# Kernel optimization log

Hardware: AMD Instinct MI355X
Metric: run time of the kernel (lower is better)

## Reference

```python
import jax, jax.numpy as jnp
import numpy as np

TEMPERATURE = 0.1
NORM_EPS = 1e-12  # matches torch F.normalize default eps


def setup_inputs() -> dict:
    key = jax.random.key(0)
    # [C crops, V=2 views, B batch, D out_dim]
    inp = jax.random.normal(key, (8, 2, 4096, 512), dtype=jnp.float32)
    return {"inp": inp}


def _ntxent_loss(inp, temperature=TEMPERATURE):
    # inp: [C, 2, B, D]
    C, V, B, D = inp.shape
    norm = jnp.linalg.norm(inp, axis=-1, keepdims=True)
    xn = inp / jnp.maximum(norm, NORM_EPS)  # l2-normalize each embedding

    # sim_all[i, b, j, v] = <xn[i,0,b], xn[j,v,b]> / temperature
    sim_all = jnp.einsum('ibd,jvbd->ibjv', xn[:, 0], xn) / temperature

    # positive logit: view-1 of the same crop i (label 0 in the original cat)
    sim_pos = sim_all[jnp.arange(C), :, jnp.arange(C), 1]  # [C, B]

    # negatives: both views of all crops j != i; mask out j == i with -inf
    same_crop = (jnp.arange(C)[:, None, None, None] == jnp.arange(C)[None, None, :, None])
    neg = jnp.where(same_crop, -jnp.inf, sim_all)  # [C, B, C, 2]

    # cross-entropy with label 0 == -log softmax over [pos, negs]
    all_logits = jnp.concatenate([sim_pos[..., None], neg.reshape(C, B, -1)], axis=-1)
    lse = jax.nn.logsumexp(all_logits, axis=-1)  # [C, B]
    loss_ib = lse - sim_pos

    # mean over crops i per sample, then mean over batch b
    return jnp.mean(loss_ib)


def reference(inp):
    return _ntxent_loss(inp)
```

## Files before the change

kernel.cpp:

```cpp
#include <hip/hip_runtime.h>
#include <hip/hip_bf16.h>
#include <math.h>

#define CC 8
#define BB 4096
#define DD 512
#define SLOT_STRIDE (BB * DD)

constexpr float INV_T    = 10.0f;
constexpr float NORM_EPS = 1e-12f;

typedef __attribute__((ext_vector_type(8))) short bf16x8;
typedef __attribute__((ext_vector_type(4))) float f32x4;

__device__ __forceinline__ short f2bf(float x) {
    union { __hip_bfloat16 h; short s; } u;
    u.h = __float2bfloat16(x);
    return u.s;
}

__global__ __launch_bounds__(256, 4)
void ntxent_mfma(const float* __restrict__ inp, float* __restrict__ partial) {
    const int lane = threadIdx.x & 63;
    const int wv   = threadIdx.x >> 6;
    const int b    = blockIdx.x * 4 + wv;
    const int slot = lane & 15;
    const int kg   = lane >> 4;

    const float4* p4 = reinterpret_cast<const float4*>(
        inp + (size_t)slot * SLOT_STRIDE + (size_t)b * DD);

    f32x4 acc0 = {0.f, 0.f, 0.f, 0.f};
    f32x4 acc1 = {0.f, 0.f, 0.f, 0.f};
    float n2a = 0.f, n2b = 0.f;

#pragma unroll
    for (int tt = 0; tt < 8; ++tt) {
#pragma unroll
        for (int h = 0; h < 2; ++h) {
            const int t = 2 * tt + h;
            const float4 lo = p4[8 * t + kg];
            const float4 hi = p4[8 * t + 4 + kg];
            n2a = fmaf(lo.x, lo.x, n2a);
            n2a = fmaf(lo.y, lo.y, n2a);
            n2a = fmaf(lo.z, lo.z, n2a);
            n2a = fmaf(lo.w, lo.w, n2a);
            n2b = fmaf(hi.x, hi.x, n2b);
            n2b = fmaf(hi.y, hi.y, n2b);
            n2b = fmaf(hi.z, hi.z, n2b);
            n2b = fmaf(hi.w, hi.w, n2b);
            bf16x8 f;
            f[0] = f2bf(lo.x); f[1] = f2bf(lo.y); f[2] = f2bf(lo.z); f[3] = f2bf(lo.w);
            f[4] = f2bf(hi.x); f[5] = f2bf(hi.y); f[6] = f2bf(hi.z); f[7] = f2bf(hi.w);
            if (h == 0)
                acc0 = __builtin_amdgcn_mfma_f32_16x16x32_bf16(f, f, acc0, 0, 0, 0);
            else
                acc1 = __builtin_amdgcn_mfma_f32_16x16x32_bf16(f, f, acc1, 0, 0, 0);
        }
    }
    const f32x4 acc = acc0 + acc1;

    float n2 = n2a + n2b;
    n2 += __shfl_xor(n2, 16);
    n2 += __shfl_xor(n2, 32);
    const float invc = 1.0f / fmaxf(sqrtf(n2), NORM_EPS);

    const float inv0 = __shfl(invc, 4 * kg);
    const float inv2 = __shfl(invc, 4 * kg + 2);

    const float s0 = acc[0] * inv0 * invc * INV_T;
    const float s2 = acc[2] * inv2 * invc * INV_T;

    const int gbase = kg << 4;
    const float pos0 = __shfl(s0, gbase + 4 * kg + 1);
    const float pos1 = __shfl(s2, gbase + 4 * kg + 3);

    float e0 = ((slot >> 1) == 2 * kg)     ? 0.f : __expf(s0 - pos0);
    float e1 = ((slot >> 1) == 2 * kg + 1) ? 0.f : __expf(s2 - pos1);
#pragma unroll
    for (int m = 1; m < 16; m <<= 1) {
        e0 += __shfl_xor(e0, m);
        e1 += __shfl_xor(e1, m);
    }
    float l = __logf(1.0f + e0) + __logf(1.0f + e1);
    l += __shfl_xor(l, 16);
    l += __shfl_xor(l, 32);

    __shared__ float s_wsum[4];
    if (lane == 0) s_wsum[wv] = l;
    __syncthreads();
    if (threadIdx.x == 0)
        partial[blockIdx.x] = s_wsum[0] + s_wsum[1] + s_wsum[2] + s_wsum[3];
}

__global__ __launch_bounds__(256)
void ntxent_reduce(const float* __restrict__ partial, float* __restrict__ out) {
    const int tid = threadIdx.x;
    const float4 v = reinterpret_cast<const float4*>(partial)[tid];
    float s = v.x + v.y + v.z + v.w;
#pragma unroll
    for (int m = 1; m < 64; m <<= 1) s += __shfl_xor(s, m);
    __shared__ float ws[4];
    if ((tid & 63) == 0) ws[tid >> 6] = s;
    __syncthreads();
    if (tid == 0)
        out[0] = (ws[0] + ws[1] + ws[2] + ws[3]) * (1.0f / (float)(CC * BB));
}

extern "C" void kernel_launch(void* const* d_in, const int* in_sizes, int n_in,
                              void* d_out, int out_size, void* d_ws, size_t ws_size,
                              hipStream_t stream) {
    const float* inp = (const float*)d_in[0];
    float* out      = (float*)d_out;
    float* partial  = (float*)d_ws;
    ntxent_mfma<<<dim3(BB / 4), dim3(256), 0, stream>>>(inp, partial);
    ntxent_reduce<<<dim3(1), dim3(256), 0, stream>>>(partial, out);
}
```

Baseline: 29.68 us.

## Split each sample's K-dimension across two waves and combine partial MFMA sums via LDS

Each sample is now handled by two waves that each cover half of the 512-dim reduction, doubling the grid to 2048 blocks and the wave count. Partial MFMA accumulators and squared norms go through LDS and are combined by the first wave, which then runs the softmax/logsumexp epilogue. The intent is more memory-level parallelism and shorter per-wave load chains in this bandwidth-bound kernel. The cost is an extra barrier and LDS exchange, half the waves sitting idle during the epilogue, and a reduce kernel that reads twice as many partials.

```diff
diff --git a/kernel.cpp b/kernel.cpp
--- a/kernel.cpp
+++ b/kernel.cpp
@@ -6,6 +6,7 @@
 #define BB 4096
 #define DD 512
 #define SLOT_STRIDE (BB * DD)
+#define NBLK (BB / 2)
 
 constexpr float INV_T    = 10.0f;
 constexpr float NORM_EPS = 1e-12f;
@@ -19,28 +20,30 @@
     return u.s;
 }
 
-__global__ __launch_bounds__(256, 4)
+__global__ __launch_bounds__(256, 8)
 void ntxent_mfma(const float* __restrict__ inp, float* __restrict__ partial) {
     const int lane = threadIdx.x & 63;
-    const int wv   = threadIdx.x >> 6;
-    const int b    = blockIdx.x * 4 + wv;
+    const int wv2  = (threadIdx.x >> 6) & 1;
+    const int pr   = threadIdx.x >> 7;
+    const int b    = blockIdx.x * 2 + pr;
     const int slot = lane & 15;
     const int kg   = lane >> 4;
 
-    const float4* p4 = reinterpret_cast<const float4*>(
+    const f32x4* p4 = reinterpret_cast<const f32x4*>(
         inp + (size_t)slot * SLOT_STRIDE + (size_t)b * DD);
 
     f32x4 acc0 = {0.f, 0.f, 0.f, 0.f};
     f32x4 acc1 = {0.f, 0.f, 0.f, 0.f};
     float n2a = 0.f, n2b = 0.f;
 
+    const int t0 = 8 * wv2;
 #pragma unroll
-    for (int tt = 0; tt < 8; ++tt) {
+    for (int tt = 0; tt < 4; ++tt) {
 #pragma unroll
         for (int h = 0; h < 2; ++h) {
-            const int t = 2 * tt + h;
-            const float4 lo = p4[8 * t + kg];
-            const float4 hi = p4[8 * t + 4 + kg];
+            const int t = t0 + 2 * tt + h;
+            const f32x4 lo = p4[8 * t + kg];
+            const f32x4 hi = p4[8 * t + 4 + kg];
             n2a = fmaf(lo.x, lo.x, n2a);
             n2a = fmaf(lo.y, lo.y, n2a);
             n2a = fmaf(lo.z, lo.z, n2a);
@@ -58,46 +61,65 @@
                 acc1 = __builtin_amdgcn_mfma_f32_16x16x32_bf16(f, f, acc1, 0, 0, 0);
         }
     }
-    const f32x4 acc = acc0 + acc1;
+    f32x4 acc = acc0 + acc1;
+    float n2  = n2a + n2b;
 
-    float n2 = n2a + n2b;
-    n2 += __shfl_xor(n2, 16);
-    n2 += __shfl_xor(n2, 32);
-    const float invc = 1.0f / fmaxf(sqrtf(n2), NORM_EPS);
+    __shared__ float lds[2][64][5];
+    __shared__ float s_wsum[2];
+    if (wv2 == 1) {
+        lds[pr][lane][0] = acc[0];
+        lds[pr][lane][1] = acc[1];
+        lds[pr][lane][2] = acc[2];
+        lds[pr][lane][3] = acc[3];
+        lds[pr][lane][4] = n2;
+    }
+    __syncthreads();
 
-    const float inv0 = __shfl(invc, 4 * kg);
-    const float inv2 = __shfl(invc, 4 * kg + 2);
+    if (wv2 == 0) {
+        acc[0] += lds[pr][lane][0];
+        acc[1] += lds[pr][lane][1];
+        acc[2] += lds[pr][lane][2];
+        acc[3] += lds[pr][lane][3];
+        n2     += lds[pr][lane][4];
 
-    const float s0 = acc[0] * inv0 * invc * INV_T;
-    const float s2 = acc[2] * inv2 * invc * INV_T;
+        n2 += __shfl_xor(n2, 16);
+        n2 += __shfl_xor(n2, 32);
+        const float invc = 1.0f / fmaxf(sqrtf(n2), NORM_EPS);
 
-    const int gbase = kg << 4;
-    const float pos0 = __shfl(s0, gbase + 4 * kg + 1);
-    const float pos1 = __shfl(s2, gbase + 4 * kg + 3);
+        const float inv0 = __shfl(invc, 4 * kg);
+        const float inv2 = __shfl(invc, 4 * kg + 2);
 
-    float e0 = ((slot >> 1) == 2 * kg)     ? 0.f : __expf(s0 - pos0);
-    float e1 = ((slot >> 1) == 2 * kg + 1) ? 0.f : __expf(s2 - pos1);
+        const float s0 = acc[0] * inv0 * invc * INV_T;
+        const float s2 = acc[2] * inv2 * invc * INV_T;
+
+        const int gbase = kg << 4;
+        const float pos0 = __shfl(s0, gbase + 4 * kg + 1);
+        const float pos1 = __shfl(s2, gbase + 4 * kg + 3);
+
+        float e0 = ((slot >> 1) == 2 * kg)     ? 0.f : __expf(s0 - pos0);
+        float e1 = ((slot >> 1) == 2 * kg + 1) ? 0.f : __expf(s2 - pos1);
 #pragma unroll
-    for (int m = 1; m < 16; m <<= 1) {
-        e0 += __shfl_xor(e0, m);
-        e1 += __shfl_xor(e1, m);
+        for (int m = 1; m < 16; m <<= 1) {
+            e0 += __shfl_xor(e0, m);
+            e1 += __shfl_xor(e1, m);
+        }
+        float l = __logf(1.0f + e0) + __logf(1.0f + e1);
+        l += __shfl_xor(l, 16);
+        l += __shfl_xor(l, 32);
+
+        if (lane == 0) s_wsum[pr] = l;
     }
-    float l = __logf(1.0f + e0) + __logf(1.0f + e1);
-    l += __shfl_xor(l, 16);
-    l += __shfl_xor(l, 32);
-
-    __shared__ float s_wsum[4];
-    if (lane == 0) s_wsum[wv] = l;
     __syncthreads();
-    if (threadIdx.x == 0)
-        partial[blockIdx.x] = s_wsum[0] + s_wsum[1] + s_wsum[2] + s_wsum[3];
+    if (threadIdx.x == 0) partial[blockIdx.x] = s_wsum[0] + s_wsum[1];
 }
 
 __global__ __launch_bounds__(256)
 void ntxent_reduce(const float* __restrict__ partial, float* __restrict__ out) {
     const int tid = threadIdx.x;
-    const float4 v = reinterpret_cast<const float4*>(partial)[tid];
-    float s = v.x + v.y + v.z + v.w;
+    const f32x4* pv = reinterpret_cast<const f32x4*>(partial);
+    const f32x4 v0 = pv[tid];
+    const f32x4 v1 = pv[tid + 256];
+    float s = v0.x + v0.y + v0.z + v0.w + v1.x + v1.y + v1.z + v1.w;
 #pragma unroll
     for (int m = 1; m < 64; m <<= 1) s += __shfl_xor(s, m);
     __shared__ float ws[4];
@@ -113,6 +135,6 @@
     const float* inp = (const float*)d_in[0];
     float* out      = (float*)d_out;
     float* partial  = (float*)d_ws;
-    ntxent_mfma<<<dim3(BB / 4), dim3(256), 0, stream>>>(inp, partial);
+    ntxent_mfma<<<dim3(NBLK), dim3(256), 0, stream>>>(inp, partial);
     ntxent_reduce<<<dim3(1), dim3(256), 0, stream>>>(partial, out);
 }
```

Result: slower. 31.84 us (+7.3%).
